# Performance work log

Measured on AMD Instinct MI355X. Metric: run time of the kernel, lower is better.

Reference implementation:

```python
import jax, jax.numpy as jnp
import numpy as np

CHARS_SIZE = 10000
HIDDEN = 1024
OUTPUT = 100
BATCH = 4096
MAXLEN = 2048


def setup_inputs() -> dict:
    key = jax.random.key(0)
    k1, k2, k3 = jax.random.split(key, 3)
    words_t = jax.random.randint(k1, (BATCH, MAXLEN), 0, CHARS_SIZE, dtype=jnp.int64 if jax.config.jax_enable_x64 else jnp.int32)
    # Xavier-uniform init like the torch module
    lim1 = float(np.sqrt(6.0 / (CHARS_SIZE + HIDDEN)))
    lim2 = float(np.sqrt(6.0 / (HIDDEN + OUTPUT)))
    W1 = jax.random.uniform(k2, (HIDDEN, CHARS_SIZE), jnp.float32, -lim1, lim1)
    b1 = jnp.zeros((HIDDEN,), jnp.float32)
    W2 = jax.random.uniform(k3, (OUTPUT, HIDDEN), jnp.float32, -lim2, lim2)
    b2 = jnp.zeros((OUTPUT,), jnp.float32)
    return {"words_t": words_t, "W1": W1, "b1": b1, "W2": W2, "b2": b2}


def reference(words_t, W1, b1, W2, b2):
    batch, maxlen = words_t.shape
    # Direct scatter-add histogram: equivalent to one-hot(batch,maxlen,chars)
    # summed over maxlen, without materializing the dense one-hot tensor.
    hist = jnp.zeros((batch, CHARS_SIZE), jnp.float32)
    rows = jnp.arange(batch)[:, None]  # (batch, 1) broadcast over maxlen
    hist = hist.at[rows, words_t].add(1.0)
    hid = hist @ W1.T + b1            # (batch, hidden)
    out = hid @ W2.T + b2             # (batch, output)
    return out
```

## Files before the change

### kernel.cpp

```cpp
#include <hip/hip_runtime.h>
#include <stdint.h>

#define CHARS   10000
#define KPAD    10240
#define HIDDEN  1024
#define OUTPUT  100
#define OPAD    128
#define BATCH   4096
#define MAXLEN  2048

typedef __bf16 bf16_t;
typedef __bf16 bf16x8 __attribute__((ext_vector_type(8)));
typedef __bf16 bf16x4 __attribute__((ext_vector_type(4)));
typedef float  f32x4  __attribute__((ext_vector_type(4)));
typedef uint32_t u32x4 __attribute__((ext_vector_type(4)));

__device__ __forceinline__ void gload16(const bf16_t* g, bf16_t* l) {
    __builtin_amdgcn_global_load_lds(
        (__attribute__((address_space(1))) void*)const_cast<bf16_t*>(g),
        (__attribute__((address_space(3))) void*)l, 16, 0, 0);
}

__global__ void k_prep(const float* __restrict__ W1, bf16_t* __restrict__ W1b,
                       const float* __restrict__ W2, float* __restrict__ W2T,
                       const float* __restrict__ b1, float* __restrict__ hid) {
    const int bid = blockIdx.x, tid = threadIdx.x;
    if (bid < 2048) {
        const int row = bid >> 1;
        const int g0  = (bid & 1) * 1280;
        for (int j = 0; j < 5; ++j) {
            int c4 = g0 + j * 256 + tid;
            bf16x4 o;
            if (c4 * 4 < CHARS) {
                f32x4 v = *(const f32x4*)(W1 + (size_t)row * CHARS + (size_t)c4 * 4);
                o[0] = (bf16_t)v[0]; o[1] = (bf16_t)v[1];
                o[2] = (bf16_t)v[2]; o[3] = (bf16_t)v[3];
            } else {
                o[0] = o[1] = o[2] = o[3] = (bf16_t)0.0f;
            }
            *(bf16x4*)(W1b + (size_t)row * KPAD + (size_t)c4 * 4) = o;
        }
    } else if (bid < 2560) {
        int i = (bid - 2048) * 256 + tid;
        int o = i & (OPAD - 1), k = i >> 7;
        W2T[i] = (o < OUTPUT) ? W2[(size_t)o * HIDDEN + k] : 0.0f;
    } else {
        const int M4 = BATCH * HIDDEN / 4;
        for (int i = (bid - 2560) * 256 + tid; i < M4; i += 2048 * 256) {
            int h4 = i & (HIDDEN / 4 - 1);
            ((f32x4*)hid)[i] = ((const f32x4*)b1)[h4];
        }
    }
}

__device__ __forceinline__ void hist_body(uint32_t* h2, const int* __restrict__ words,
                                          bf16_t* __restrict__ hist, int row,
                                          int dstRow, int tid) {
#pragma unroll
    for (int i = 0; i < KPAD / 2 / 4 / 256; ++i)
        *(u32x4*)(h2 + (i * 256 + tid) * 4) = (u32x4){0u, 0u, 0u, 0u};
    __syncthreads();
    const int* w = words + (size_t)row * MAXLEN;
#pragma unroll
    for (int i = 0; i < MAXLEN / 4 / 256; ++i) {
        int4 t4 = *(const int4*)(w + (i * 256 + tid) * 4);
        atomicAdd(&h2[t4.x >> 1], 1u << ((t4.x & 1) * 16));
        atomicAdd(&h2[t4.y >> 1], 1u << ((t4.y & 1) * 16));
        atomicAdd(&h2[t4.z >> 1], 1u << ((t4.z & 1) * 16));
        atomicAdd(&h2[t4.w >> 1], 1u << ((t4.w & 1) * 16));
    }
    __syncthreads();
    bf16_t* dst = hist + (size_t)dstRow * KPAD;
#pragma unroll
    for (int i = 0; i < KPAD / 8 / 256; ++i) {
        int j = (i * 256 + tid) * 8;
        u32x4 v = *(const u32x4*)(h2 + (j >> 1));
        bf16x8 o;
#pragma unroll
        for (int q = 0; q < 4; ++q) {
            o[2 * q]     = (bf16_t)(float)(v[q] & 0xffffu);
            o[2 * q + 1] = (bf16_t)(float)(v[q] >> 16);
        }
        *(bf16x8*)(dst + j) = o;
    }
}

__global__ void k_hist(const int* __restrict__ words, bf16_t* __restrict__ hist,
                       int rowStart) {
    __shared__ uint32_t h2[KPAD / 2];
    hist_body(h2, words, hist, rowStart + blockIdx.x, blockIdx.x, threadIdx.x);
}

__global__ void k_preph(const int* __restrict__ words, bf16_t* __restrict__ hist,
                        const float* __restrict__ W1, bf16_t* __restrict__ W1b,
                        const float* __restrict__ W2, float* __restrict__ W2T,
                        const float* __restrict__ b1, float* __restrict__ hid,
                        int initHid) {
    __shared__ uint32_t h2[KPAD / 2];
    const int bid = blockIdx.x, tid = threadIdx.x;
    if (bid < BATCH) {
        hist_body(h2, words, hist, bid, bid, tid);
    } else if (bid < BATCH + 2048) {
        const int b2i = bid - BATCH;
        const int row = b2i >> 1;
        const int g0  = (b2i & 1) * 1280;
        for (int j = 0; j < 5; ++j) {
            int c4 = g0 + j * 256 + tid;
            bf16x4 o;
            if (c4 * 4 < CHARS) {
                f32x4 v = *(const f32x4*)(W1 + (size_t)row * CHARS + (size_t)c4 * 4);
                o[0] = (bf16_t)v[0]; o[1] = (bf16_t)v[1];
                o[2] = (bf16_t)v[2]; o[3] = (bf16_t)v[3];
            } else {
                o[0] = o[1] = o[2] = o[3] = (bf16_t)0.0f;
            }
            *(bf16x4*)(W1b + (size_t)row * KPAD + (size_t)c4 * 4) = o;
        }
    } else if (bid < BATCH + 2560) {
        int i = (bid - BATCH - 2048) * 256 + tid;
        int o = i & (OPAD - 1), k = i >> 7;
        W2T[i] = (o < OUTPUT) ? W2[(size_t)o * HIDDEN + k] : 0.0f;
    } else if (initHid) {
        const int b2i = bid - BATCH - 2560;
        const int M4 = BATCH * HIDDEN / 4;
        for (int i = b2i * 256 + tid; i < M4; i += 2048 * 256) {
            int h4 = i & (HIDDEN / 4 - 1);
            ((f32x4*)hid)[i] = ((const f32x4*)b1)[h4];
        }
    }
}

template <int EPI>
__global__ void __launch_bounds__(512)
k_gemm(const bf16_t* __restrict__ A, const bf16_t* __restrict__ Bt,
       float* __restrict__ hid, float* __restrict__ extraSlabs,
       int KT, int mtiles) {
    __shared__ __attribute__((aligned(16))) bf16_t As[2][2][128 * 64];
    __shared__ __attribute__((aligned(16))) bf16_t Bs[2][2][128 * 64];

    const int nblk = gridDim.x;
    int idx = blockIdx.x;
    if ((nblk & 7) == 0) idx = (idx & 7) * (nblk >> 3) + (idx >> 3);
    const int mt = idx % mtiles;
    const int ns = idx / mtiles;
    const int m0 = mt * 256;
    const int n0 = (ns & 3) * 256;
    const int kbeg = (ns >> 2) * KT;

    const int tid  = threadIdx.x;
    const int lane = tid & 63;
    const int wave = tid >> 6;
    const int wm64 = (wave >> 2) * 64;
    const int wn32 = (wave & 3) * 32;
    const int l15  = lane & 15;
    const int hi   = lane >> 4;
    const int x3   = l15 & 7;

    int arow[4], brow[2], koff[2];
#pragma unroll
    for (int fi = 0; fi < 4; ++fi) arow[fi] = (wm64 + fi * 16 + l15) * 128;
#pragma unroll
    for (int fj = 0; fj < 2; ++fj) brow[fj] = (wn32 + fj * 16 + l15) * 128;
#pragma unroll
    for (int kk = 0; kk < 2; ++kk) koff[kk] = ((((kk << 2) | hi)) ^ x3) * 16;

    const int srow = lane >> 3;
    const int csw8 = ((lane & 7) ^ srow) * 8;
    const bf16_t* Ab = A  + (size_t)(m0 + wave * 16 + srow) * KPAD + csw8;
    const bf16_t* Bb = Bt + (size_t)(n0 + wave * 16 + srow) * KPAD + csw8;
    const int wsl = wave * 2 * 512;

    f32x4 acc[2][2][4][2] = {};
    bf16x8 Afa0[2][4], Afa1[2][4], Bfa0[2][4], Bfa1[2][4];
    bf16x8 Afb0[2][2], Afb1[2][2], Bfb0[2][2], Bfb1[2][2];

#define STAGE(SB, SOP, SH, KTILE_) do {                                        \
    int kte_ = (KTILE_); if (kte_ >= KT) kte_ = 0;             \
    const size_t kc_ = (size_t)(kbeg + kte_) * 64;                             \
    const bf16_t* gb_ = (SOP) ? Bb : Ab;                                       \
    bf16_t* lb_ = ((SOP) ? &Bs[SB][SH][0] : &As[SB][SH][0]) + wsl;             \
    gload16(gb_ + (size_t)((SH) * 128)     * KPAD + kc_, lb_);                 \
    gload16(gb_ + (size_t)((SH) * 128 + 8) * KPAD + kc_, lb_ + 512);           \
} while (0)

#define LOADA(DST, PB, HALF) do {                                              \
    const char* p_ = (const char*)&As[PB][HALF][0];                            \
    _Pragma("unroll") for (int kk = 0; kk < 2; ++kk)                           \
        _Pragma("unroll") for (int fi = 0; fi < 4; ++fi)                       \
            DST[kk][fi] = *(const bf16x8*)(p_ + arow[fi] + koff[kk]);          \
} while (0)

#define LOADB(DST, PB, HALF) do {                                              \
    const char* p_ = (const char*)&Bs[PB][HALF][0];                            \
    _Pragma("unroll") for (int kk = 0; kk < 2; ++kk)                           \
        _Pragma("unroll") for (int fj = 0; fj < 2; ++fj)                       \
            DST[kk][fj] = *(const bf16x8*)(p_ + brow[fj] + koff[kk]);          \
} while (0)

#define PHB() do {                                                             \
    __builtin_amdgcn_sched_barrier(0);                                         \
    __builtin_amdgcn_s_barrier();                                              \
    __builtin_amdgcn_sched_barrier(0);                                         \
} while (0)

#define VM4() asm volatile("s_waitcnt vmcnt(4)" ::: "memory")

#define MMQ(QI, QJ, FA, FB) do {                                               \
    __builtin_amdgcn_s_setprio(1);                                             \
    _Pragma("unroll") for (int kk = 0; kk < 2; ++kk)                           \
        _Pragma("unroll") for (int fi = 0; fi < 4; ++fi)                       \
            _Pragma("unroll") for (int fj = 0; fj < 2; ++fj)                   \
                acc[QI][QJ][fi][fj] = __builtin_amdgcn_mfma_f32_16x16x32_bf16( \
                    FA[kk][fi], FB[kk][fj], acc[QI][QJ][fi][fj], 0, 0, 0);     \
    __builtin_amdgcn_s_setprio(0);                                             \
} while (0)

    STAGE(0, 0, 0, 0);
    STAGE(0, 1, 0, 0);
    STAGE(0, 0, 1, 0);
    STAGE(0, 1, 1, 0);
    STAGE(1, 1, 0, 1);
    STAGE(1, 0, 0, 1);
    VM4();
    PHB();
    LOADA(Afa0, 0, 0);
    LOADB(Afb0, 0, 0);

    for (int kt = 0; kt < KT; kt += 2) {
        PHB();
        STAGE(1, 0, 1, kt + 1);
        LOADA(Afa1, 0, 1);
        MMQ(0, 0, Afa0, Afb0);
        VM4();
        PHB();
        STAGE(1, 1, 1, kt + 1);
        LOADB(Afb1, 0, 1);
        MMQ(1, 0, Afa1, Afb0);
        PHB();
        STAGE(0, 1, 0, kt + 2);
        MMQ(0, 1, Afa0, Afb1);
        VM4();
        PHB();
        STAGE(0, 0, 0, kt + 2);
        LOADA(Bfa0, 1, 0);
        LOADB(Bfb0, 1, 0);
        MMQ(1, 1, Afa1, Afb1);
        PHB();
        STAGE(0, 0, 1, kt + 2);
        LOADA(Bfa1, 1, 1);
        MMQ(0, 0, Bfa0, Bfb0);
        VM4();
        PHB();
        STAGE(0, 1, 1, kt + 2);
        LOADB(Bfb1, 1, 1);
        MMQ(1, 0, Bfa1, Bfb0);
        PHB();
        STAGE(1, 1, 0, kt + 3);
        MMQ(0, 1, Bfa0, Bfb1);
        VM4();
        PHB();
        STAGE(1, 0, 0, kt + 3);
        LOADA(Afa0, 0, 0);
        LOADB(Afb0, 0, 0);
        MMQ(1, 1, Bfa1, Bfb1);
    }
#undef MMQ
#undef VM4
#undef PHB
#undef LOADB
#undef LOADA
#undef STAGE

    const int er = hi * 4;
    float* dstBase;
    if (EPI == 1) {
        const int s = ns >> 2;
        dstBase = (s == 0) ? hid : extraSlabs + (size_t)(s - 1) * BATCH * HIDDEN;
    } else {
        dstBase = hid;
    }
#pragma unroll
    for (int qi = 0; qi < 2; ++qi)
#pragma unroll
    for (int qj = 0; qj < 2; ++qj)
#pragma unroll
    for (int fi = 0; fi < 4; ++fi)
#pragma unroll
    for (int fj = 0; fj < 2; ++fj) {
        float* dst = dstBase + (size_t)(m0 + qi * 128 + wm64 + fi * 16 + er) * HIDDEN
                             + (n0 + qj * 128 + wn32 + fj * 16 + l15);
#pragma unroll
        for (int r = 0; r < 4; ++r) {
            if (EPI == 1) dst[(size_t)r * HIDDEN] = acc[qi][qj][fi][fj][r];
            else          atomicAdd(dst + (size_t)r * HIDDEN, acc[qi][qj][fi][fj][r]);
        }
    }
}

__global__ void k_red(float* __restrict__ hid, const float* __restrict__ extra,
                      const float* __restrict__ b1) {
    const int N4 = BATCH * HIDDEN / 4;
    const float* e0 = extra;
    const float* e1 = extra + (size_t)BATCH * HIDDEN;
    const float* e2 = extra + (size_t)2 * BATCH * HIDDEN;
    for (int i = blockIdx.x * 256 + threadIdx.x; i < N4; i += 2048 * 256) {
        int h4 = i & (HIDDEN / 4 - 1);
        f32x4 v = ((const f32x4*)hid)[i];
        v += ((const f32x4*)b1)[h4];
        v += ((const f32x4*)e0)[i];
        v += ((const f32x4*)e1)[i];
        v += ((const f32x4*)e2)[i];
        ((f32x4*)hid)[i] = v;
    }
}

__global__ void k_out2(const float* __restrict__ hid, const float* __restrict__ W2T,
                       const float* __restrict__ b2, float* __restrict__ out) {
    __shared__ float red[4][16][OPAD];
    const int tid  = threadIdx.x;
    const int o4   = (tid & 31) * 4;
    const int slot = tid >> 5;
    const int rg   = slot >> 2;
    const int kc   = slot & 3;
    const int rbase = blockIdx.x * 16 + rg * 8;

    f32x4 acc8[8] = {};
    const int k0beg = kc * 256;
    for (int k0 = k0beg; k0 < k0beg + 256; k0 += 4) {
        f32x4 wv0 = *(const f32x4*)(W2T + (size_t)(k0 + 0) * OPAD + o4);
        f32x4 wv1 = *(const f32x4*)(W2T + (size_t)(k0 + 1) * OPAD + o4);
        f32x4 wv2 = *(const f32x4*)(W2T + (size_t)(k0 + 2) * OPAD + o4);
        f32x4 wv3 = *(const f32x4*)(W2T + (size_t)(k0 + 3) * OPAD + o4);
#pragma unroll
        for (int r = 0; r < 8; ++r) {
            f32x4 hv = *(const f32x4*)(hid + (size_t)(rbase + r) * HIDDEN + k0);
            acc8[r] += hv[0] * wv0 + hv[1] * wv1 + hv[2] * wv2 + hv[3] * wv3;
        }
    }
#pragma unroll
    for (int r = 0; r < 8; ++r)
        *(f32x4*)&red[kc][rg * 8 + r][o4] = acc8[r];
    __syncthreads();
    const int row = tid >> 4;
    const int o8  = (tid & 15) * 8;
    f32x4 s0 = {0.f, 0.f, 0.f, 0.f}, s1 = {0.f, 0.f, 0.f, 0.f};
#pragma unroll
    for (int c = 0; c < 4; ++c) {
        s0 += *(const f32x4*)&red[c][row][o8];
        s1 += *(const f32x4*)&red[c][row][o8 + 4];
    }
    float* op = out + (size_t)(blockIdx.x * 16 + row) * OUTPUT;
#pragma unroll
    for (int j = 0; j < 4; ++j) {
        if (o8 + j < OUTPUT)     op[o8 + j]     = s0[j] + b2[o8 + j];
        if (o8 + 4 + j < OUTPUT) op[o8 + 4 + j] = s1[j] + b2[o8 + 4 + j];
    }
}

__global__ void k_out(const float* __restrict__ hid, const float* __restrict__ W2T,
                      const float* __restrict__ b2, float* __restrict__ out) {
    const int tid = threadIdx.x;
    const int o4  = (tid & 31) * 4;
    const int rs  = tid >> 5;
    const int row = blockIdx.x * 8 + rs;
    const float* hrow = hid + (size_t)row * HIDDEN;
    f32x4 acc = {0.f, 0.f, 0.f, 0.f};
    for (int k0 = 0; k0 < HIDDEN; k0 += 4) {
        f32x4 hv = *(const f32x4*)(hrow + k0);
#pragma unroll
        for (int q = 0; q < 4; ++q) {
            f32x4 wv = *(const f32x4*)(W2T + (size_t)(k0 + q) * OPAD + o4);
            acc += hv[q] * wv;
        }
    }
    if (o4 < OUTPUT) {
        float* op = out + (size_t)row * OUTPUT + o4;
#pragma unroll
        for (int q = 0; q < 4; ++q)
            op[q] = acc[q] + b2[o4 + q];
    }
}

static inline int pick_S(int mtiles) {
    const int cands[10] = {80, 40, 20, 16, 10, 8, 5, 4, 2, 1};
    for (int i = 0; i < 10; ++i)
        if (mtiles * 4 * cands[i] <= 256) return cands[i];
    return 1;
}

extern "C" void kernel_launch(void* const* d_in, const int* in_sizes, int n_in,
                              void* d_out, int out_size, void* d_ws, size_t ws_size,
                              hipStream_t stream) {
    (void)in_sizes; (void)n_in; (void)out_size;
    const int*   words = (const int*)d_in[0];
    const float* W1    = (const float*)d_in[1];
    const float* b1    = (const float*)d_in[2];
    const float* W2    = (const float*)d_in[3];
    const float* b2    = (const float*)d_in[4];
    float* out = (float*)d_out;

    char* ws = (char*)d_ws;
    size_t off = 0;
    bf16_t* W1b  = (bf16_t*)(ws + off); off += (size_t)HIDDEN * KPAD * sizeof(bf16_t);
    float*  hid  = (float*) (ws + off); off += (size_t)BATCH * HIDDEN * sizeof(float);
    float*  W2T  = (float*) (ws + off); off += (size_t)HIDDEN * OPAD * sizeof(float);
    const size_t slabBytes = (size_t)BATCH * HIDDEN * sizeof(float);
    const size_t histBytes = (size_t)BATCH * KPAD * sizeof(bf16_t);

    if (ws_size >= off + 3 * slabBytes + histBytes) {
        float* extra = (float*)(ws + off);
        bf16_t* histC = (bf16_t*)(ws + off + 3 * slabBytes);
        k_preph<<<dim3(BATCH + 4608), dim3(256), 0, stream>>>(
            words, histC, W1, W1b, W2, W2T, b1, hid, 0);
        int mtiles = BATCH / 256;
        int S = 4;
        int KT = (KPAD / 64) / S;
        k_gemm<1><<<dim3(mtiles * 4 * S), dim3(512), 0, stream>>>(
            histC, W1b, hid, extra, KT, mtiles);
        k_red<<<dim3(2048), dim3(256), 0, stream>>>(hid, extra, b1);
        k_out2<<<dim3(BATCH / 16), dim3(256), 0, stream>>>(hid, W2T, b2, out);
    } else {
        bf16_t* histC = (bf16_t*)(ws + off);
        size_t rem = (ws_size > off) ? (ws_size - off) : 0;
        int chunkRows = (int)(rem / ((size_t)KPAD * sizeof(bf16_t)));
        chunkRows = (chunkRows / 256) * 256;
        if (chunkRows > BATCH) chunkRows = BATCH;
        if (chunkRows < 256)   chunkRows = 256;

        if (chunkRows >= BATCH) {
            k_preph<<<dim3(BATCH + 4608), dim3(256), 0, stream>>>(
                words, histC, W1, W1b, W2, W2T, b1, hid, 1);
            int mtiles = BATCH / 256;
            int S = pick_S(mtiles);
            int KT = (KPAD / 64) / S;
            k_gemm<0><<<dim3(mtiles * 4 * S), dim3(512), 0, stream>>>(
                histC, W1b, hid, nullptr, KT, mtiles);
        } else {
            k_prep<<<dim3(4608), dim3(256), 0, stream>>>(W1, W1b, W2, W2T, b1, hid);
            for (int r0 = 0; r0 < BATCH; r0 += chunkRows) {
                int rows = BATCH - r0;
                if (rows > chunkRows) rows = chunkRows;
                k_hist<<<dim3(rows), dim3(256), 0, stream>>>(words, histC, r0);
                int mtiles = rows / 256;
                int S = pick_S(mtiles);
                int KT = (KPAD / 64) / S;
                k_gemm<0><<<dim3(mtiles * 4 * S), dim3(512), 0, stream>>>(
                    histC, W1b, hid + (size_t)r0 * HIDDEN, nullptr, KT, mtiles);
            }
        }
        k_out<<<dim3(BATCH / 8), dim3(256), 0, stream>>>(hid, W2T, b2, out);
    }
}
```

Measured before the change: 256.1 us.

## Replace split-K GEMM plus reduction with full-K 128x128 tile GEMM

The main path previously ran a 256x256-tile GEMM split four ways along K, writing partial results into extra fp32 slabs, then ran a separate reduction kernel that added the slabs and the bias. It now launches a new full-K kernel with 128x128 tiles, 256 blocks and a simple double-buffered LDS pipeline, and adds the bias in the epilogue. This removes the slab writes, the reduction pass and the workspace they needed. In exchange each block does a long serial K loop with less MFMA work per loaded byte and a less elaborate pipeline. The fallback path is also simplified to always use chunked histogram passes.

Result: slower. 331.0 us (+29.3%).

```diff
diff --git a/kernel.cpp b/kernel.cpp
--- a/kernel.cpp
+++ b/kernel.cpp
@@ -130,11 +130,105 @@
     }
 }
 
-template <int EPI>
+__global__ void __launch_bounds__(512, 4)
+k_gemm1(const bf16_t* __restrict__ A, const bf16_t* __restrict__ Bt,
+        float* __restrict__ hid, const float* __restrict__ b1) {
+    __shared__ __attribute__((aligned(16))) bf16_t As[2][128 * 64];
+    __shared__ __attribute__((aligned(16))) bf16_t Bs[2][128 * 64];
+
+    const int nblk = gridDim.x;
+    int idx = blockIdx.x;
+    idx = (idx & 7) * (nblk >> 3) + (idx >> 3);
+    const int mt = idx & 31;
+    const int nt = idx >> 5;
+    const int m0 = mt * 128;
+    const int n0 = nt * 128;
+
+    const int tid  = threadIdx.x;
+    const int lane = tid & 63;
+    const int wave = tid >> 6;
+    const int wm32 = (wave >> 1) * 32;
+    const int wn64 = (wave & 1) * 64;
+    const int l15  = lane & 15;
+    const int hi   = lane >> 4;
+    const int x3   = l15 & 7;
+
+    int arow[2], brow[4], koff[2];
+#pragma unroll
+    for (int fi = 0; fi < 2; ++fi) arow[fi] = (wm32 + fi * 16 + l15) * 128;
+#pragma unroll
+    for (int fj = 0; fj < 4; ++fj) brow[fj] = (wn64 + fj * 16 + l15) * 128;
+#pragma unroll
+    for (int kk = 0; kk < 2; ++kk) koff[kk] = ((((kk << 2) | hi)) ^ x3) * 16;
+
+    const int srow = lane >> 3;
+    const int csw8 = ((lane & 7) ^ srow) * 8;
+    const bf16_t* Ab = A  + (size_t)(m0 + wave * 16 + srow) * KPAD + csw8;
+    const bf16_t* Bb = Bt + (size_t)(n0 + wave * 16 + srow) * KPAD + csw8;
+    const int wsl = wave * 1024;
+
+    f32x4 acc[2][4] = {};
+
+#define STAGE4(BUF, KTILE_) do {                                               \
+    int kte_ = (KTILE_); if (kte_ >= 160) kte_ = 0;            \
+    const size_t kc_ = (size_t)kte_ * 64;                                      \
+    gload16(Ab + kc_,                      &As[BUF][0] + wsl);                 \
+    gload16(Ab + (size_t)8 * KPAD + kc_,   &As[BUF][0] + wsl + 512);           \
+    gload16(Bb + kc_,                      &Bs[BUF][0] + wsl);                 \
+    gload16(Bb + (size_t)8 * KPAD + kc_,   &Bs[BUF][0] + wsl + 512);           \
+} while (0)
+
+#define BODY(CUR, NXT, KTN) do {                                               \
+    STAGE4(NXT, KTN);                                                          \
+    bf16x8 af_[2][2], bf_[2][4];                                               \
+    _Pragma("unroll") for (int kk = 0; kk < 2; ++kk) {                         \
+        _Pragma("unroll") for (int fi = 0; fi < 2; ++fi)                       \
+            af_[kk][fi] = *(const bf16x8*)((const char*)&As[CUR][0] +          \
+                                           arow[fi] + koff[kk]);               \
+        _Pragma("unroll") for (int fj = 0; fj < 4; ++fj)                       \
+            bf_[kk][fj] = *(const bf16x8*)((const char*)&Bs[CUR][0] +          \
+                                           brow[fj] + koff[kk]);               \
+    }                                                                          \
+    _Pragma("unroll") for (int kk = 0; kk < 2; ++kk)                           \
+        _Pragma("unroll") for (int fi = 0; fi < 2; ++fi)                       \
+            _Pragma("unroll") for (int fj = 0; fj < 4; ++fj)                   \
+                acc[fi][fj] = __builtin_amdgcn_mfma_f32_16x16x32_bf16(         \
+                    af_[kk][fi], bf_[kk][fj], acc[fi][fj], 0, 0, 0);           \
+    asm volatile("s_waitcnt vmcnt(0)" ::: "memory");                           \
+    __builtin_amdgcn_sched_barrier(0);                                         \
+    __builtin_amdgcn_s_barrier();                                              \
+    __builtin_amdgcn_sched_barrier(0);                                         \
+} while (0)
+
+    STAGE4(0, 0);
+    asm volatile("s_waitcnt vmcnt(0)" ::: "memory");
+    __builtin_amdgcn_s_barrier();
+    __builtin_amdgcn_sched_barrier(0);
+
+    for (int kt = 0; kt < 160; kt += 2) {
+        BODY(0, 1, kt + 1);
+        BODY(1, 0, kt + 2);
+    }
+#undef BODY
+#undef STAGE4
+
+    const int er = hi * 4;
+#pragma unroll
+    for (int fi = 0; fi < 2; ++fi)
+#pragma unroll
+    for (int fj = 0; fj < 4; ++fj) {
+        const int col = n0 + wn64 + fj * 16 + l15;
+        const float bv = b1[col];
+        float* dst = hid + (size_t)(m0 + wm32 + fi * 16 + er) * HIDDEN + col;
+#pragma unroll
+        for (int r = 0; r < 4; ++r)
+            dst[(size_t)r * HIDDEN] = acc[fi][fj][r] + bv;
+    }
+}
+
 __global__ void __launch_bounds__(512)
 k_gemm(const bf16_t* __restrict__ A, const bf16_t* __restrict__ Bt,
-       float* __restrict__ hid, float* __restrict__ extraSlabs,
-       int KT, int mtiles) {
+       float* __restrict__ hid, int KT, int mtiles) {
     __shared__ __attribute__((aligned(16))) bf16_t As[2][2][128 * 64];
     __shared__ __attribute__((aligned(16))) bf16_t Bs[2][2][128 * 64];
 
@@ -175,7 +269,7 @@
     bf16x8 Afb0[2][2], Afb1[2][2], Bfb0[2][2], Bfb1[2][2];
 
 #define STAGE(SB, SOP, SH, KTILE_) do {                                        \
-    int kte_ = (KTILE_); if (kte_ >= KT) kte_ = 0;             \
+    int kte_ = (KTILE_); if (kte_ >= KT) kte_ = 0;                             \
     const size_t kc_ = (size_t)(kbeg + kte_) * 64;                             \
     const bf16_t* gb_ = (SOP) ? Bb : Ab;                                       \
     bf16_t* lb_ = ((SOP) ? &Bs[SB][SH][0] : &As[SB][SH][0]) + wsl;             \
@@ -272,13 +366,6 @@
 #undef STAGE
 
     const int er = hi * 4;
-    float* dstBase;
-    if (EPI == 1) {
-        const int s = ns >> 2;
-        dstBase = (s == 0) ? hid : extraSlabs + (size_t)(s - 1) * BATCH * HIDDEN;
-    } else {
-        dstBase = hid;
-    }
 #pragma unroll
     for (int qi = 0; qi < 2; ++qi)
 #pragma unroll
@@ -287,30 +374,11 @@
     for (int fi = 0; fi < 4; ++fi)
 #pragma unroll
     for (int fj = 0; fj < 2; ++fj) {
-        float* dst = dstBase + (size_t)(m0 + qi * 128 + wm64 + fi * 16 + er) * HIDDEN
-                             + (n0 + qj * 128 + wn32 + fj * 16 + l15);
-#pragma unroll
-        for (int r = 0; r < 4; ++r) {
-            if (EPI == 1) dst[(size_t)r * HIDDEN] = acc[qi][qj][fi][fj][r];
-            else          atomicAdd(dst + (size_t)r * HIDDEN, acc[qi][qj][fi][fj][r]);
-        }
-    }
-}
-
-__global__ void k_red(float* __restrict__ hid, const float* __restrict__ extra,
-                      const float* __restrict__ b1) {
-    const int N4 = BATCH * HIDDEN / 4;
-    const float* e0 = extra;
-    const float* e1 = extra + (size_t)BATCH * HIDDEN;
-    const float* e2 = extra + (size_t)2 * BATCH * HIDDEN;
-    for (int i = blockIdx.x * 256 + threadIdx.x; i < N4; i += 2048 * 256) {
-        int h4 = i & (HIDDEN / 4 - 1);
-        f32x4 v = ((const f32x4*)hid)[i];
-        v += ((const f32x4*)b1)[h4];
-        v += ((const f32x4*)e0)[i];
-        v += ((const f32x4*)e1)[i];
-        v += ((const f32x4*)e2)[i];
-        ((f32x4*)hid)[i] = v;
+        float* dst = hid + (size_t)(m0 + qi * 128 + wm64 + fi * 16 + er) * HIDDEN
+                         + (n0 + qj * 128 + wn32 + fj * 16 + l15);
+#pragma unroll
+        for (int r = 0; r < 4; ++r)
+            atomicAdd(dst + (size_t)r * HIDDEN, acc[qi][qj][fi][fj][r]);
     }
 }
 
@@ -404,20 +472,13 @@
     bf16_t* W1b  = (bf16_t*)(ws + off); off += (size_t)HIDDEN * KPAD * sizeof(bf16_t);
     float*  hid  = (float*) (ws + off); off += (size_t)BATCH * HIDDEN * sizeof(float);
     float*  W2T  = (float*) (ws + off); off += (size_t)HIDDEN * OPAD * sizeof(float);
-    const size_t slabBytes = (size_t)BATCH * HIDDEN * sizeof(float);
     const size_t histBytes = (size_t)BATCH * KPAD * sizeof(bf16_t);
 
-    if (ws_size >= off + 3 * slabBytes + histBytes) {
-        float* extra = (float*)(ws + off);
-        bf16_t* histC = (bf16_t*)(ws + off + 3 * slabBytes);
+    if (ws_size >= off + histBytes) {
+        bf16_t* histC = (bf16_t*)(ws + off);
         k_preph<<<dim3(BATCH + 4608), dim3(256), 0, stream>>>(
             words, histC, W1, W1b, W2, W2T, b1, hid, 0);
-        int mtiles = BATCH / 256;
-        int S = 4;
-        int KT = (KPAD / 64) / S;
-        k_gemm<1><<<dim3(mtiles * 4 * S), dim3(512), 0, stream>>>(
-            histC, W1b, hid, extra, KT, mtiles);
-        k_red<<<dim3(2048), dim3(256), 0, stream>>>(hid, extra, b1);
+        k_gemm1<<<dim3(256), dim3(512), 0, stream>>>(histC, W1b, hid, b1);
         k_out2<<<dim3(BATCH / 16), dim3(256), 0, stream>>>(hid, W2T, b2, out);
     } else {
         bf16_t* histC = (bf16_t*)(ws + off);
@@ -427,26 +488,16 @@
         if (chunkRows > BATCH) chunkRows = BATCH;
         if (chunkRows < 256)   chunkRows = 256;
 
-        if (chunkRows >= BATCH) {
-            k_preph<<<dim3(BATCH + 4608), dim3(256), 0, stream>>>(
-                words, histC, W1, W1b, W2, W2T, b1, hid, 1);
-            int mtiles = BATCH / 256;
+        k_prep<<<dim3(4608), dim3(256), 0, stream>>>(W1, W1b, W2, W2T, b1, hid);
+        for (int r0 = 0; r0 < BATCH; r0 += chunkRows) {
+            int rows = BATCH - r0;
+            if (rows > chunkRows) rows = chunkRows;
+            k_hist<<<dim3(rows), dim3(256), 0, stream>>>(words, histC, r0);
+            int mtiles = rows / 256;
             int S = pick_S(mtiles);
             int KT = (KPAD / 64) / S;
-            k_gemm<0><<<dim3(mtiles * 4 * S), dim3(512), 0, stream>>>(
-                histC, W1b, hid, nullptr, KT, mtiles);
-        } else {
-            k_prep<<<dim3(4608), dim3(256), 0, stream>>>(W1, W1b, W2, W2T, b1, hid);
-            for (int r0 = 0; r0 < BATCH; r0 += chunkRows) {
-                int rows = BATCH - r0;
-                if (rows > chunkRows) rows = chunkRows;
-                k_hist<<<dim3(rows), dim3(256), 0, stream>>>(words, histC, r0);
-                int mtiles = rows / 256;
-                int S = pick_S(mtiles);
-                int KT = (KPAD / 64) / S;
-                k_gemm<0><<<dim3(mtiles * 4 * S), dim3(512), 0, stream>>>(
-                    histC, W1b, hid + (size_t)r0 * HIDDEN, nullptr, KT, mtiles);
-            }
+            k_gemm<<<dim3(mtiles * 4 * S), dim3(512), 0, stream>>>(
+                histC, W1b, hid + (size_t)r0 * HIDDEN, KT, mtiles);
         }
         k_out<<<dim3(BATCH / 8), dim3(256), 0, stream>>>(hid, W2T, b2, out);
     }
```
